# Kernel optimization log

Hardware: AMD Instinct MI355X
Metric: run time of the kernel (lower is better)

## Reference

```python
import jax, jax.numpy as jnp
import numpy as np

B, D, NT, H, K = 4096, 112, 200, 512, 10
HID = 512
IN = 3 * D + NT + 1   # GRU input size = 537
M0 = H + 3 * D + NT   # MLP first-layer input = 1048


def setup_inputs() -> dict:
    key = jax.random.key(0)
    ks = jax.random.split(key, 9)
    def w(k, shape, fan):
        return jax.random.normal(k, shape, jnp.float32) / np.sqrt(fan).astype(np.float32)
    return {
        "z": jax.random.normal(ks[0], (B, D), jnp.float32),
        "c": jax.random.normal(ks[1], (B, D + NT), jnp.float32),
        "b": jax.random.uniform(ks[2], (B, D), jnp.float32),
        "m": jax.random.uniform(ks[3], (B, D), jnp.float32),
        "Wih": w(ks[4], (IN, 3 * H), IN),
        "Whh": w(ks[5], (H, 3 * H), H),
        "bih": jnp.zeros((3 * H,), jnp.float32),
        "bhh": jnp.zeros((3 * H,), jnp.float32),
        "W0": w(ks[6], (M0, HID), M0),
        "b0": jnp.zeros((HID,), jnp.float32),
        "W1": w(ks[7], (HID, HID), HID),
        "b1": jnp.zeros((HID,), jnp.float32),
        "W2": w(ks[8], (HID, 3 * K), HID),
        "b2": jnp.zeros((3 * K,), jnp.float32),
    }


def reference(z, c, b, m, Wih, Whh, bih, bhh, W0, b0, W1, b1, W2, b2):
    """AutoReg.logp: autoregressive GRU + MLP mixture-density head, gaussian base."""
    Bn = z.shape[0]
    const = jnp.concatenate([c, b, m], axis=1)          # [B, 3D+NT] fixed per step
    gi_const = const @ Wih[1:] + bih                    # input-proj of constant part
    w_z = Wih[0]                                        # [3H] weight for scalar z_t
    mlp_const = const @ W0[H:] + b0                     # const part of first MLP layer
    W0h = W0[:H]
    # teacher-forced previous-z sequence: z_0 = -1, then z[:, t-1]
    z_prev = jnp.concatenate([-jnp.ones((Bn, 1), z.dtype), z[:, :-1]], axis=1).T  # [D, B]

    def step(h, zt):  # h: [B,H], zt: [B]
        gi = zt[:, None] * w_z + gi_const               # [B, 3H]
        gh = h @ Whh + bhh
        ir, iz, inn = jnp.split(gi, 3, axis=1)
        hr, hz, hn = jnp.split(gh, 3, axis=1)
        r = jax.nn.sigmoid(ir + hr)
        u = jax.nn.sigmoid(iz + hz)
        n = jnp.tanh(inn + r * hn)
        h2 = (1.0 - u) * n + u * h                      # torch GRU update
        a = jnp.tanh(h2 @ W0h + mlp_const)              # Linear + Tanh on [h||c||b||m]
        a = jnp.tanh(a @ W1 + b1)
        p = a @ W2 + b2                                 # [B, 3K] mixture params
        return h2, p

    h0 = jnp.zeros((Bn, H), z.dtype)
    _, ps = jax.lax.scan(step, h0, z_prev)              # ps: [D, B, 3K]
    params = jnp.transpose(ps, (1, 0, 2))               # [B, D, 3K]

    logits, means, lsig = jnp.split(params, 3, axis=-1)
    sig = jnp.exp(lsig)
    t = z[..., None]
    log_norm = -lsig - 0.5 * np.float32(np.log(2.0 * np.pi))
    log_kern = -0.5 * jnp.square((t - means) / sig)
    ll = jax.nn.logsumexp(log_kern + log_norm + logits, axis=-1) \
         - jax.nn.logsumexp(logits, axis=-1)            # [B, D]

    query = m * (1.0 - b)
    mask = -jnp.sort(-query, axis=1)                    # descending sort values
    return jnp.sum(ll * mask, axis=1)                   # [B]
```

## Files before the change

### kernel.cpp

```cpp
#include <hip/hip_runtime.h>
#include <hip/hip_bf16.h>
#include <float.h>
#include <math.h>

#define BN   4096
#define DD   112
#define HH   512
#define G3   1536
#define CW   536
#define HIDD 512

typedef __attribute__((ext_vector_type(8))) short short8;
typedef __attribute__((ext_vector_type(4))) float float4v;

__device__ __forceinline__ unsigned short f2bf(float x) {
    __hip_bfloat16 h = __float2bfloat16(x);
    return *(unsigned short*)&h;
}

__global__ void build_const(const float* __restrict__ c, const float* __restrict__ b,
                            const float* __restrict__ m, float* __restrict__ out) {
    int idx = blockIdx.x * blockDim.x + threadIdx.x;
    if (idx >= BN * CW) return;
    int row = idx / CW, col = idx - row * CW;
    float v;
    if (col < 312)      v = c[row * 312 + col];
    else if (col < 424) v = b[row * 112 + (col - 312)];
    else                v = m[row * 112 + (col - 424)];
    out[idx] = v;
}

__global__ __launch_bounds__(256) void gemm_bias(const float* __restrict__ A,
        const float* __restrict__ W, const float* __restrict__ bias,
        float* __restrict__ C, int N) {
    __shared__ float As[8][64];
    __shared__ float Ws[8][64];
    const int tid = threadIdx.x;
    const int tx = tid & 15, ty = tid >> 4;
    const int rowBase = blockIdx.x * 64, colBase = blockIdx.y * 64;
    float acc[4][4] = {};
    for (int kb = 0; kb < CW; kb += 8) {
        int l = tid * 2;
        {
            int i = l >> 3, j = l & 7;
            As[j][i] = A[(rowBase + i) * CW + kb + j];
            int i2 = (l + 1) >> 3, j2 = (l + 1) & 7;
            As[j2][i2] = A[(rowBase + i2) * CW + kb + j2];
        }
        {
            int j = l >> 6, n = l & 63;
            Ws[j][n] = W[(kb + j) * N + colBase + n];
            int j2 = (l + 1) >> 6, n2 = (l + 1) & 63;
            Ws[j2][n2] = W[(kb + j2) * N + colBase + n2];
        }
        __syncthreads();
#pragma unroll
        for (int k = 0; k < 8; ++k) {
            float av[4], wv[4];
#pragma unroll
            for (int i = 0; i < 4; ++i) av[i] = As[k][ty * 4 + i];
#pragma unroll
            for (int j = 0; j < 4; ++j) wv[j] = Ws[k][tx * 4 + j];
#pragma unroll
            for (int i = 0; i < 4; ++i)
#pragma unroll
                for (int j = 0; j < 4; ++j) acc[i][j] += av[i] * wv[j];
        }
        __syncthreads();
    }
#pragma unroll
    for (int i = 0; i < 4; ++i) {
        int r = rowBase + ty * 4 + i;
#pragma unroll
        for (int j = 0; j < 4; ++j) {
            int cc = colBase + tx * 4 + j;
            C[r * N + cc] = acc[i][j] + bias[cc];
        }
    }
}

__global__ void sort_mask(const float* __restrict__ b, const float* __restrict__ m,
                          float* __restrict__ maskbuf) {
    __shared__ float s[128];
    const int row = blockIdx.x, t = threadIdx.x;
    float v = -FLT_MAX;
    if (t < DD) v = m[row * DD + t] * (1.0f - b[row * DD + t]);
    s[t] = v;
    __syncthreads();
    for (int k = 2; k <= 128; k <<= 1) {
        for (int j = k >> 1; j > 0; j >>= 1) {
            int ixj = t ^ j;
            if (ixj > t) {
                bool up = ((t & k) == 0);
                float a = s[t], bb = s[ixj];
                if ((a > bb) == up) { s[t] = bb; s[ixj] = a; }
            }
            __syncthreads();
        }
    }
    if (t < DD) maskbuf[row * DD + t] = s[127 - t];
}

__global__ void pack_w(const float* __restrict__ src, unsigned short* __restrict__ dst,
                       int kchunks, int ldn, int ncols) {
    int bid = blockIdx.x;
    int nt = bid / kchunks, kc = bid - nt * kchunks;
    int lane = threadIdx.x;
    int quad = lane >> 4, l16 = lane & 15;
    int n = nt * 16 + l16;
    unsigned short v[8];
#pragma unroll
    for (int j = 0; j < 8; ++j) {
        int k = kc * 32 + quad * 8 + j;
        float f = (n < ncols) ? src[(size_t)k * ldn + n] : 0.0f;
        v[j] = f2bf(f);
    }
    unsigned short* p = dst + ((size_t)bid * 64 + lane) * 8;
#pragma unroll
    for (int j = 0; j < 8; ++j) p[j] = v[j];
}

__global__ __launch_bounds__(1024, 4) void gru_mfma(
    const float* __restrict__ z, const float* __restrict__ Wih,
    const float* __restrict__ bhh, const float* __restrict__ b1,
    const float* __restrict__ b2,
    const float* __restrict__ gi_const, const float* __restrict__ mlp_const,
    const float* __restrict__ maskbuf,
    const unsigned short* __restrict__ WhhP, const unsigned short* __restrict__ W0hP,
    const unsigned short* __restrict__ W1P, const unsigned short* __restrict__ W2P,
    float* __restrict__ out)
{
    __shared__ unsigned short h_bf[16 * 520];
    __shared__ unsigned short a_bf[16 * 520];
    __shared__ float pp[16 * 512];
    __shared__ float zbuf[113 * 16];
    __shared__ float mbuf[16 * 112];

    const int tid = threadIdx.x;
    const int wave = tid >> 6, lane = tid & 63;
    const int quad = lane >> 4, l16 = lane & 15;
    const int pr = tid >> 5, pc = tid & 31;
    const int rowBase = blockIdx.x * 16;

    for (int idx = tid; idx < 16 * 520; idx += 1024) h_bf[idx] = 0;
    for (int idx = tid; idx < 113 * 16; idx += 1024) {
        int tt = idx >> 4, r = idx & 15;
        zbuf[idx] = (tt == 0) ? -1.0f : z[(rowBase + r) * DD + tt - 1];
    }
    for (int idx = tid; idx < 16 * 112; idx += 1024) {
        int r = idx / DD, tt = idx - r * DD;
        mbuf[idx] = maskbuf[(rowBase + r) * DD + tt];
    }

    int hcol[2];
    float wz0[2], wz1[2], wz2[2], bh2r[2], b1c[2];
    float gic0[2][4], gic1[2][4], gic2[2][4], mlc[2][4];
    float h_own[2][4];
#pragma unroll
    for (int i = 0; i < 2; ++i) {
        int tile = wave + 16 * i;
        int hc = tile * 16 + l16;
        hcol[i] = hc;
        wz0[i] = Wih[hc]; wz1[i] = Wih[512 + hc]; wz2[i] = Wih[1024 + hc];
        float bh0 = bhh[hc], bh1 = bhh[512 + hc];
        bh2r[i] = bhh[1024 + hc];
        b1c[i] = b1[hc];
#pragma unroll
        for (int rg = 0; rg < 4; ++rg) {
            int m = quad * 4 + rg;
            const float* g = gi_const + (size_t)(rowBase + m) * G3;
            gic0[i][rg] = g[hc] + bh0;
            gic1[i][rg] = g[512 + hc] + bh1;
            gic2[i][rg] = g[1024 + hc];
            mlc[i][rg] = mlp_const[(size_t)(rowBase + m) * HIDD + hc];
            h_own[i][rg] = 0.0f;
        }
    }
    const float b2v = (pc < 30) ? b2[pc] : 0.0f;
    const int ppbase = (pc >> 4) * 256 + ((pr >> 2) * 16 + (pc & 15)) * 4 + (pr & 3);

    const short8* WhhF = (const short8*)WhhP;
    const short8* W0hF = (const short8*)W0hP;
    const short8* W1F  = (const short8*)W1P;
    const short8* W2F  = (const short8*)W2P;

    float llacc = 0.0f;
    __syncthreads();

    for (int t = 0; t < DD; ++t) {
        float4v accR[2], accU[2], accN[2];
#pragma unroll
        for (int i = 0; i < 2; ++i) {
            accR[i] = (float4v){gic0[i][0], gic0[i][1], gic0[i][2], gic0[i][3]};
            accU[i] = (float4v){gic1[i][0], gic1[i][1], gic1[i][2], gic1[i][3]};
            accN[i] = (float4v){0.f, 0.f, 0.f, 0.f};
        }
#pragma unroll 4
        for (int kc = 0; kc < 16; ++kc) {
            short8 af = *(const short8*)&h_bf[l16 * 520 + kc * 32 + quad * 8];
#pragma unroll
            for (int i = 0; i < 2; ++i) {
                int tile = wave + 16 * i;
                accR[i] = __builtin_amdgcn_mfma_f32_16x16x32_bf16(af, WhhF[(tile * 16 + kc) * 64 + lane], accR[i], 0, 0, 0);
                accU[i] = __builtin_amdgcn_mfma_f32_16x16x32_bf16(af, WhhF[((tile + 32) * 16 + kc) * 64 + lane], accU[i], 0, 0, 0);
                accN[i] = __builtin_amdgcn_mfma_f32_16x16x32_bf16(af, WhhF[((tile + 64) * 16 + kc) * 64 + lane], accN[i], 0, 0, 0);
            }
        }
        __syncthreads();
#pragma unroll
        for (int i = 0; i < 2; ++i) {
#pragma unroll
            for (int rg = 0; rg < 4; ++rg) {
                int m = quad * 4 + rg;
                float zt = zbuf[t * 16 + m];
                float r = 1.0f / (1.0f + __expf(-(accR[i][rg] + zt * wz0[i])));
                float u = 1.0f / (1.0f + __expf(-(accU[i][rg] + zt * wz1[i])));
                float xn = gic2[i][rg] + zt * wz2[i] + r * (accN[i][rg] + bh2r[i]);
                float n = 1.0f - 2.0f / (__expf(2.0f * xn) + 1.0f);
                float h2 = (1.0f - u) * n + u * h_own[i][rg];
                h_own[i][rg] = h2;
                h_bf[m * 520 + hcol[i]] = f2bf(h2);
            }
        }
        __syncthreads();
        float4v acc1[2];
#pragma unroll
        for (int i = 0; i < 2; ++i) acc1[i] = (float4v){mlc[i][0], mlc[i][1], mlc[i][2], mlc[i][3]};
#pragma unroll 4
        for (int kc = 0; kc < 16; ++kc) {
            short8 af = *(const short8*)&h_bf[l16 * 520 + kc * 32 + quad * 8];
#pragma unroll
            for (int i = 0; i < 2; ++i)
                acc1[i] = __builtin_amdgcn_mfma_f32_16x16x32_bf16(af, W0hF[((wave + 16 * i) * 16 + kc) * 64 + lane], acc1[i], 0, 0, 0);
        }
#pragma unroll
        for (int i = 0; i < 2; ++i)
#pragma unroll
            for (int rg = 0; rg < 4; ++rg) {
                int m = quad * 4 + rg;
                float x = acc1[i][rg];
                a_bf[m * 520 + hcol[i]] = f2bf(1.0f - 2.0f / (__expf(2.0f * x) + 1.0f));
            }
        __syncthreads();
        float4v acc2[2];
#pragma unroll
        for (int i = 0; i < 2; ++i) acc2[i] = (float4v){b1c[i], b1c[i], b1c[i], b1c[i]};
#pragma unroll 4
        for (int kc = 0; kc < 16; ++kc) {
            short8 af = *(const short8*)&a_bf[l16 * 520 + kc * 32 + quad * 8];
#pragma unroll
            for (int i = 0; i < 2; ++i)
                acc2[i] = __builtin_amdgcn_mfma_f32_16x16x32_bf16(af, W1F[((wave + 16 * i) * 16 + kc) * 64 + lane], acc2[i], 0, 0, 0);
        }
        __syncthreads();
#pragma unroll
        for (int i = 0; i < 2; ++i)
#pragma unroll
            for (int rg = 0; rg < 4; ++rg) {
                int m = quad * 4 + rg;
                float x = acc2[i][rg];
                a_bf[m * 520 + hcol[i]] = f2bf(1.0f - 2.0f / (__expf(2.0f * x) + 1.0f));
            }
        __syncthreads();
        {
            int kc = wave;
            short8 af = *(const short8*)&a_bf[l16 * 520 + kc * 32 + quad * 8];
            float4v ap0 = (float4v){0.f, 0.f, 0.f, 0.f}, ap1 = (float4v){0.f, 0.f, 0.f, 0.f};
            ap0 = __builtin_amdgcn_mfma_f32_16x16x32_bf16(af, W2F[(0 * 16 + kc) * 64 + lane], ap0, 0, 0, 0);
            ap1 = __builtin_amdgcn_mfma_f32_16x16x32_bf16(af, W2F[(1 * 16 + kc) * 64 + lane], ap1, 0, 0, 0);
#pragma unroll
            for (int rg = 0; rg < 4; ++rg) {
                pp[wave * 512 + 0 * 256 + lane * 4 + rg] = ap0[rg];
                pp[wave * 512 + 1 * 256 + lane * 4 + rg] = ap1[rg];
            }
        }
        __syncthreads();
        if (wave < 8) {
            float pv = b2v;
#pragma unroll
            for (int w = 0; w < 16; ++w) pv += pp[w * 512 + ppbase];
            const int half = lane & 32;
            float meanv = __shfl(pv, half + ((pc + 10) & 31), 64);
            float lsigv = __shfl(pv, half + ((pc + 20) & 31), 64);
            float e1, e2;
            if (pc < 10) {
                float ztar = zbuf[(t + 1) * 16 + pr];
                float invs = __expf(-lsigv);
                float dd = (ztar - meanv) * invs;
                e1 = -0.5f * dd * dd - lsigv - 0.91893853320467274f + pv;
                e2 = pv;
            } else { e1 = -FLT_MAX; e2 = -FLT_MAX; }
            float m1 = e1, m2 = e2;
#pragma unroll
            for (int off = 16; off > 0; off >>= 1) {
                m1 = fmaxf(m1, __shfl_xor(m1, off, 64));
                m2 = fmaxf(m2, __shfl_xor(m2, off, 64));
            }
            float s1 = (pc < 10) ? __expf(e1 - m1) : 0.0f;
            float s2 = (pc < 10) ? __expf(e2 - m2) : 0.0f;
#pragma unroll
            for (int off = 16; off > 0; off >>= 1) {
                s1 += __shfl_xor(s1, off, 64);
                s2 += __shfl_xor(s2, off, 64);
            }
            float ll = (m1 + __logf(s1)) - (m2 + __logf(s2));
            llacc += ll * mbuf[pr * 112 + t];
        }
    }
    if (wave < 8 && pc == 0) out[rowBase + pr] = llacc;
}

extern "C" void kernel_launch(void* const* d_in, const int* in_sizes, int n_in,
                              void* d_out, int out_size, void* d_ws, size_t ws_size,
                              hipStream_t stream) {
    const float* z   = (const float*)d_in[0];
    const float* c   = (const float*)d_in[1];
    const float* b   = (const float*)d_in[2];
    const float* m   = (const float*)d_in[3];
    const float* Wih = (const float*)d_in[4];
    const float* Whh = (const float*)d_in[5];
    const float* bih = (const float*)d_in[6];
    const float* bhh = (const float*)d_in[7];
    const float* W0  = (const float*)d_in[8];
    const float* b0  = (const float*)d_in[9];
    const float* W1  = (const float*)d_in[10];
    const float* b1  = (const float*)d_in[11];
    const float* W2  = (const float*)d_in[12];
    const float* b2  = (const float*)d_in[13];
    float* out = (float*)d_out;

    float* ws        = (float*)d_ws;
    float* constbuf  = ws;
    float* gi_const  = constbuf + (size_t)BN * CW;
    float* mlp_const = gi_const + (size_t)BN * G3;
    float* maskbuf   = mlp_const + (size_t)BN * HIDD;
    unsigned short* WhhP = (unsigned short*)(maskbuf + (size_t)BN * DD);
    unsigned short* W0hP = WhhP + (size_t)96 * 16 * 512;
    unsigned short* W1P  = W0hP + (size_t)32 * 16 * 512;
    unsigned short* W2P  = W1P  + (size_t)32 * 16 * 512;

    build_const<<<(BN * CW + 255) / 256, 256, 0, stream>>>(c, b, m, constbuf);
    dim3 g1(BN / 64, G3 / 64);
    gemm_bias<<<g1, 256, 0, stream>>>(constbuf, Wih + G3, bih, gi_const, G3);
    dim3 g2(BN / 64, HIDD / 64);
    gemm_bias<<<g2, 256, 0, stream>>>(constbuf, W0 + (size_t)HH * HIDD, b0, mlp_const, HIDD);
    sort_mask<<<BN, 128, 0, stream>>>(b, m, maskbuf);

    pack_w<<<96 * 16, 64, 0, stream>>>(Whh, WhhP, 16, G3, G3);
    pack_w<<<32 * 16, 64, 0, stream>>>(W0,  W0hP, 16, HIDD, HIDD);
    pack_w<<<32 * 16, 64, 0, stream>>>(W1,  W1P,  16, HIDD, HIDD);
    pack_w<<<2 * 16, 64, 0, stream>>>(W2,  W2P,  16, 30, 30);

    gru_mfma<<<BN / 16, 1024, 0, stream>>>(z, Wih, bhh, b1, b2, gi_const, mlp_const,
                                           maskbuf, WhhP, W0hP, W1P, W2P, out);
}
```

Measured before the change: 3.149 ms.

## Batch MLP head over two GRU timesteps to reuse weight fragments

The MLP head no longer depends on the recurrence, so the kernel now runs two GRU steps back to back into ping-pong hidden buffers. It then evaluates the MLP layers for both timesteps together, with each loaded W0h/W1 fragment feeding two MFMAs. The W2 projection and the mixture log-likelihood are split across all 16 waves, covering two timesteps, and partial sums are merged at the end. This halves global/L2 weight traffic and the barrier count for the MLP stages. The cost is more registers and LDS, plus an extra barrier per iteration.

```diff
diff --git a/kernel.cpp b/kernel.cpp
--- a/kernel.cpp
+++ b/kernel.cpp
@@ -130,8 +130,9 @@
     const unsigned short* __restrict__ W1P, const unsigned short* __restrict__ W2P,
     float* __restrict__ out)
 {
-    __shared__ unsigned short h_bf[16 * 520];
-    __shared__ unsigned short a_bf[16 * 520];
+    __shared__ unsigned short h_bf0[16 * 520];
+    __shared__ unsigned short h_bf1[16 * 520];
+    __shared__ unsigned short a_bf[32 * 520];
     __shared__ float pp[16 * 512];
     __shared__ float zbuf[113 * 16];
     __shared__ float mbuf[16 * 112];
@@ -142,7 +143,7 @@
     const int pr = tid >> 5, pc = tid & 31;
     const int rowBase = blockIdx.x * 16;
 
-    for (int idx = tid; idx < 16 * 520; idx += 1024) h_bf[idx] = 0;
+    for (int idx = tid; idx < 16 * 520; idx += 1024) h_bf0[idx] = 0;
     for (int idx = tid; idx < 113 * 16; idx += 1024) {
         int tt = idx >> 4, r = idx & 15;
         zbuf[idx] = (tt == 0) ? -1.0f : z[(rowBase + r) * DD + tt - 1];
@@ -177,7 +178,9 @@
         }
     }
     const float b2v = (pc < 30) ? b2[pc] : 0.0f;
-    const int ppbase = (pc >> 4) * 256 + ((pr >> 2) * 16 + (pc & 15)) * 4 + (pr & 3);
+    const int mdn_mt = pr >> 4, mdn_m = pr & 15;
+    const int ppofs = (mdn_mt * 8) * 512 + (pc >> 4) * 256
+                      + ((mdn_m >> 2) * 16 + (pc & 15)) * 4 + (mdn_m & 3);
 
     const short8* WhhF = (const short8*)WhhP;
     const short8* W0hF = (const short8*)W0hP;
@@ -187,87 +190,113 @@
     float llacc = 0.0f;
     __syncthreads();
 
-    for (int t = 0; t < DD; ++t) {
-        float4v accR[2], accU[2], accN[2];
-#pragma unroll
-        for (int i = 0; i < 2; ++i) {
-            accR[i] = (float4v){gic0[i][0], gic0[i][1], gic0[i][2], gic0[i][3]};
-            accU[i] = (float4v){gic1[i][0], gic1[i][1], gic1[i][2], gic1[i][3]};
-            accN[i] = (float4v){0.f, 0.f, 0.f, 0.f};
-        }
+    for (int t = 0; t < DD; t += 2) {
+#pragma unroll
+        for (int step = 0; step < 2; ++step) {
+            const unsigned short* hsrc = step == 0 ? h_bf0 : h_bf1;
+            unsigned short* hdst = step == 0 ? h_bf1 : h_bf0;
+            float4v accR[2], accU[2], accN[2];
+#pragma unroll
+            for (int i = 0; i < 2; ++i) {
+                accR[i] = (float4v){gic0[i][0], gic0[i][1], gic0[i][2], gic0[i][3]};
+                accU[i] = (float4v){gic1[i][0], gic1[i][1], gic1[i][2], gic1[i][3]};
+                accN[i] = (float4v){0.f, 0.f, 0.f, 0.f};
+            }
+#pragma unroll 4
+            for (int kc = 0; kc < 16; ++kc) {
+                short8 af = *(const short8*)&hsrc[l16 * 520 + kc * 32 + quad * 8];
+#pragma unroll
+                for (int i = 0; i < 2; ++i) {
+                    int tile = wave + 16 * i;
+                    accR[i] = __builtin_amdgcn_mfma_f32_16x16x32_bf16(af, WhhF[(tile * 16 + kc) * 64 + lane], accR[i], 0, 0, 0);
+                    accU[i] = __builtin_amdgcn_mfma_f32_16x16x32_bf16(af, WhhF[((tile + 32) * 16 + kc) * 64 + lane], accU[i], 0, 0, 0);
+                    accN[i] = __builtin_amdgcn_mfma_f32_16x16x32_bf16(af, WhhF[((tile + 64) * 16 + kc) * 64 + lane], accN[i], 0, 0, 0);
+                }
+            }
+#pragma unroll
+            for (int i = 0; i < 2; ++i) {
+#pragma unroll
+                for (int rg = 0; rg < 4; ++rg) {
+                    int m = quad * 4 + rg;
+                    float zt = zbuf[(t + step) * 16 + m];
+                    float r = 1.0f / (1.0f + __expf(-(accR[i][rg] + zt * wz0[i])));
+                    float u = 1.0f / (1.0f + __expf(-(accU[i][rg] + zt * wz1[i])));
+                    float xn = gic2[i][rg] + zt * wz2[i] + r * (accN[i][rg] + bh2r[i]);
+                    float n = 1.0f - 2.0f / (__expf(2.0f * xn) + 1.0f);
+                    float h2 = (1.0f - u) * n + u * h_own[i][rg];
+                    h_own[i][rg] = h2;
+                    hdst[m * 520 + hcol[i]] = f2bf(h2);
+                }
+            }
+            __syncthreads();
+        }
+        float4v acc1[2][2];
+#pragma unroll
+        for (int i = 0; i < 2; ++i)
+#pragma unroll
+            for (int mt = 0; mt < 2; ++mt)
+                acc1[i][mt] = (float4v){mlc[i][0], mlc[i][1], mlc[i][2], mlc[i][3]};
 #pragma unroll 4
         for (int kc = 0; kc < 16; ++kc) {
-            short8 af = *(const short8*)&h_bf[l16 * 520 + kc * 32 + quad * 8];
+            short8 af0 = *(const short8*)&h_bf1[l16 * 520 + kc * 32 + quad * 8];
+            short8 af1 = *(const short8*)&h_bf0[l16 * 520 + kc * 32 + quad * 8];
 #pragma unroll
             for (int i = 0; i < 2; ++i) {
-                int tile = wave + 16 * i;
-                accR[i] = __builtin_amdgcn_mfma_f32_16x16x32_bf16(af, WhhF[(tile * 16 + kc) * 64 + lane], accR[i], 0, 0, 0);
-                accU[i] = __builtin_amdgcn_mfma_f32_16x16x32_bf16(af, WhhF[((tile + 32) * 16 + kc) * 64 + lane], accU[i], 0, 0, 0);
-                accN[i] = __builtin_amdgcn_mfma_f32_16x16x32_bf16(af, WhhF[((tile + 64) * 16 + kc) * 64 + lane], accN[i], 0, 0, 0);
-            }
-        }
-        __syncthreads();
-#pragma unroll
-        for (int i = 0; i < 2; ++i) {
-#pragma unroll
-            for (int rg = 0; rg < 4; ++rg) {
-                int m = quad * 4 + rg;
-                float zt = zbuf[t * 16 + m];
-                float r = 1.0f / (1.0f + __expf(-(accR[i][rg] + zt * wz0[i])));
-                float u = 1.0f / (1.0f + __expf(-(accU[i][rg] + zt * wz1[i])));
-                float xn = gic2[i][rg] + zt * wz2[i] + r * (accN[i][rg] + bh2r[i]);
-                float n = 1.0f - 2.0f / (__expf(2.0f * xn) + 1.0f);
-                float h2 = (1.0f - u) * n + u * h_own[i][rg];
-                h_own[i][rg] = h2;
-                h_bf[m * 520 + hcol[i]] = f2bf(h2);
-            }
-        }
-        __syncthreads();
-        float4v acc1[2];
-#pragma unroll
-        for (int i = 0; i < 2; ++i) acc1[i] = (float4v){mlc[i][0], mlc[i][1], mlc[i][2], mlc[i][3]};
+                short8 bf = W0hF[((wave + 16 * i) * 16 + kc) * 64 + lane];
+                acc1[i][0] = __builtin_amdgcn_mfma_f32_16x16x32_bf16(af0, bf, acc1[i][0], 0, 0, 0);
+                acc1[i][1] = __builtin_amdgcn_mfma_f32_16x16x32_bf16(af1, bf, acc1[i][1], 0, 0, 0);
+            }
+        }
+#pragma unroll
+        for (int i = 0; i < 2; ++i)
+#pragma unroll
+            for (int mt = 0; mt < 2; ++mt)
+#pragma unroll
+                for (int rg = 0; rg < 4; ++rg) {
+                    int m = quad * 4 + rg;
+                    float x = acc1[i][mt][rg];
+                    a_bf[(mt * 16 + m) * 520 + hcol[i]] = f2bf(1.0f - 2.0f / (__expf(2.0f * x) + 1.0f));
+                }
+        __syncthreads();
+        float4v acc2[2][2];
+#pragma unroll
+        for (int i = 0; i < 2; ++i)
+#pragma unroll
+            for (int mt = 0; mt < 2; ++mt)
+                acc2[i][mt] = (float4v){b1c[i], b1c[i], b1c[i], b1c[i]};
 #pragma unroll 4
         for (int kc = 0; kc < 16; ++kc) {
-            short8 af = *(const short8*)&h_bf[l16 * 520 + kc * 32 + quad * 8];
-#pragma unroll
-            for (int i = 0; i < 2; ++i)
-                acc1[i] = __builtin_amdgcn_mfma_f32_16x16x32_bf16(af, W0hF[((wave + 16 * i) * 16 + kc) * 64 + lane], acc1[i], 0, 0, 0);
-        }
+            short8 af0 = *(const short8*)&a_bf[l16 * 520 + kc * 32 + quad * 8];
+            short8 af1 = *(const short8*)&a_bf[(16 + l16) * 520 + kc * 32 + quad * 8];
+#pragma unroll
+            for (int i = 0; i < 2; ++i) {
+                short8 bf = W1F[((wave + 16 * i) * 16 + kc) * 64 + lane];
+                acc2[i][0] = __builtin_amdgcn_mfma_f32_16x16x32_bf16(af0, bf, acc2[i][0], 0, 0, 0);
+                acc2[i][1] = __builtin_amdgcn_mfma_f32_16x16x32_bf16(af1, bf, acc2[i][1], 0, 0, 0);
+            }
+        }
+        __syncthreads();
 #pragma unroll
         for (int i = 0; i < 2; ++i)
 #pragma unroll
-            for (int rg = 0; rg < 4; ++rg) {
-                int m = quad * 4 + rg;
-                float x = acc1[i][rg];
-                a_bf[m * 520 + hcol[i]] = f2bf(1.0f - 2.0f / (__expf(2.0f * x) + 1.0f));
-            }
-        __syncthreads();
-        float4v acc2[2];
-#pragma unroll
-        for (int i = 0; i < 2; ++i) acc2[i] = (float4v){b1c[i], b1c[i], b1c[i], b1c[i]};
-#pragma unroll 4
-        for (int kc = 0; kc < 16; ++kc) {
-            short8 af = *(const short8*)&a_bf[l16 * 520 + kc * 32 + quad * 8];
-#pragma unroll
-            for (int i = 0; i < 2; ++i)
-                acc2[i] = __builtin_amdgcn_mfma_f32_16x16x32_bf16(af, W1F[((wave + 16 * i) * 16 + kc) * 64 + lane], acc2[i], 0, 0, 0);
-        }
-        __syncthreads();
-#pragma unroll
-        for (int i = 0; i < 2; ++i)
-#pragma unroll
-            for (int rg = 0; rg < 4; ++rg) {
-                int m = quad * 4 + rg;
-                float x = acc2[i][rg];
-                a_bf[m * 520 + hcol[i]] = f2bf(1.0f - 2.0f / (__expf(2.0f * x) + 1.0f));
-            }
+            for (int mt = 0; mt < 2; ++mt)
+#pragma unroll
+                for (int rg = 0; rg < 4; ++rg) {
+                    int m = quad * 4 + rg;
+                    float x = acc2[i][mt][rg];
+                    a_bf[(mt * 16 + m) * 520 + hcol[i]] = f2bf(1.0f - 2.0f / (__expf(2.0f * x) + 1.0f));
+                }
         __syncthreads();
         {
-            int kc = wave;
-            short8 af = *(const short8*)&a_bf[l16 * 520 + kc * 32 + quad * 8];
+            const int mtw = wave >> 3;
             float4v ap0 = (float4v){0.f, 0.f, 0.f, 0.f}, ap1 = (float4v){0.f, 0.f, 0.f, 0.f};
-            ap0 = __builtin_amdgcn_mfma_f32_16x16x32_bf16(af, W2F[(0 * 16 + kc) * 64 + lane], ap0, 0, 0, 0);
-            ap1 = __builtin_amdgcn_mfma_f32_16x16x32_bf16(af, W2F[(1 * 16 + kc) * 64 + lane], ap1, 0, 0, 0);
+#pragma unroll
+            for (int kk = 0; kk < 2; ++kk) {
+                int kc = (wave & 7) * 2 + kk;
+                short8 af = *(const short8*)&a_bf[(mtw * 16 + l16) * 520 + kc * 32 + quad * 8];
+                ap0 = __builtin_amdgcn_mfma_f32_16x16x32_bf16(af, W2F[(0 * 16 + kc) * 64 + lane], ap0, 0, 0, 0);
+                ap1 = __builtin_amdgcn_mfma_f32_16x16x32_bf16(af, W2F[(1 * 16 + kc) * 64 + lane], ap1, 0, 0, 0);
+            }
 #pragma unroll
             for (int rg = 0; rg < 4; ++rg) {
                 pp[wave * 512 + 0 * 256 + lane * 4 + rg] = ap0[rg];
@@ -275,16 +304,16 @@
             }
         }
         __syncthreads();
-        if (wave < 8) {
+        {
             float pv = b2v;
 #pragma unroll
-            for (int w = 0; w < 16; ++w) pv += pp[w * 512 + ppbase];
+            for (int w = 0; w < 8; ++w) pv += pp[ppofs + w * 512];
             const int half = lane & 32;
             float meanv = __shfl(pv, half + ((pc + 10) & 31), 64);
             float lsigv = __shfl(pv, half + ((pc + 20) & 31), 64);
             float e1, e2;
             if (pc < 10) {
-                float ztar = zbuf[(t + 1) * 16 + pr];
+                float ztar = zbuf[(t + mdn_mt + 1) * 16 + mdn_m];
                 float invs = __expf(-lsigv);
                 float dd = (ztar - meanv) * invs;
                 e1 = -0.5f * dd * dd - lsigv - 0.91893853320467274f + pv;
@@ -304,10 +333,13 @@
                 s2 += __shfl_xor(s2, off, 64);
             }
             float ll = (m1 + __logf(s1)) - (m2 + __logf(s2));
-            llacc += ll * mbuf[pr * 112 + t];
-        }
-    }
-    if (wave < 8 && pc == 0) out[rowBase + pr] = llacc;
+            llacc += ll * mbuf[mdn_m * 112 + t + mdn_mt];
+        }
+        __syncthreads();
+    }
+    if (pc == 0) pp[pr] = llacc;
+    __syncthreads();
+    if (tid < 16) out[rowBase + tid] = pp[tid] + pp[16 + tid];
 }
 
 extern "C" void kernel_launch(void* const* d_in, const int* in_sizes, int n_in,
```

Result: slower. 4.530 ms (+43.9%).

## Split GRU recurrence from MLP head and batch head over time steps

Applied to the files above, without the earlier changes.

Splits the fused per-step kernel into two. A recurrence-only kernel handles 32 rows per block, reuses each Whh fragment across two M-tiles, reads pre-swizzled gate constants (with bhh folded in) and writes bf16 hidden states to a workspace buffer. A separate head kernel then runs the MLP and mixture-density log-likelihood on all timesteps in parallel, accumulating into the output with atomics. This takes the serial MLP work off the recurrence's critical path and raises parallelism, at the cost of about 470MB of extra global traffic for the hidden states, a workspace-size-dependent fallback, and float atomics that make the summation order nondeterministic.

```diff
diff --git a/kernel.cpp b/kernel.cpp
--- a/kernel.cpp
+++ b/kernel.cpp
@@ -79,6 +79,62 @@
     }
 }
 
+__global__ __launch_bounds__(256) void gemm_gicP(const float* __restrict__ A,
+        const float* __restrict__ W, const float* __restrict__ bih,
+        const float* __restrict__ bhh, float* __restrict__ gicP) {
+    const int N = G3;
+    __shared__ float As[8][64];
+    __shared__ float Ws[8][64];
+    const int tid = threadIdx.x;
+    const int tx = tid & 15, ty = tid >> 4;
+    const int rowBase = blockIdx.x * 64, colBase = blockIdx.y * 64;
+    float acc[4][4] = {};
+    for (int kb = 0; kb < CW; kb += 8) {
+        int l = tid * 2;
+        {
+            int i = l >> 3, j = l & 7;
+            As[j][i] = A[(rowBase + i) * CW + kb + j];
+            int i2 = (l + 1) >> 3, j2 = (l + 1) & 7;
+            As[j2][i2] = A[(rowBase + i2) * CW + kb + j2];
+        }
+        {
+            int j = l >> 6, n = l & 63;
+            Ws[j][n] = W[(kb + j) * N + colBase + n];
+            int j2 = (l + 1) >> 6, n2 = (l + 1) & 63;
+            Ws[j2][n2] = W[(kb + j2) * N + colBase + n2];
+        }
+        __syncthreads();
+#pragma unroll
+        for (int k = 0; k < 8; ++k) {
+            float av[4], wv[4];
+#pragma unroll
+            for (int i = 0; i < 4; ++i) av[i] = As[k][ty * 4 + i];
+#pragma unroll
+            for (int j = 0; j < 4; ++j) wv[j] = Ws[k][tx * 4 + j];
+#pragma unroll
+            for (int i = 0; i < 4; ++i)
+#pragma unroll
+                for (int j = 0; j < 4; ++j) acc[i][j] += av[i] * wv[j];
+        }
+        __syncthreads();
+    }
+#pragma unroll
+    for (int i = 0; i < 4; ++i) {
+        int r = rowBase + ty * 4 + i;
+        int ablock = r >> 5, mrem = r & 31, mt = mrem >> 4, mm = mrem & 15;
+        int quad = mm >> 2, rg = mm & 3;
+#pragma unroll
+        for (int j = 0; j < 4; ++j) {
+            int cc = colBase + tx * 4 + j;
+            int g = cc >> 9, nrem = cc & 511, tile = nrem >> 4, l16 = nrem & 15;
+            int wv = tile & 15, ii = tile >> 4;
+            size_t off = ((((size_t)(ablock * 16 + wv) * 2 + ii) * 2 + mt) * 3 + g) * 256
+                         + (quad * 16 + l16) * 4 + rg;
+            gicP[off] = acc[i][j] + bih[cc] + ((g < 2) ? bhh[cc] : 0.0f);
+        }
+    }
+}
+
 __global__ void sort_mask(const float* __restrict__ b, const float* __restrict__ m,
                           float* __restrict__ maskbuf) {
     __shared__ float s[128];
@@ -120,7 +176,270 @@
     for (int j = 0; j < 8; ++j) p[j] = v[j];
 }
 
-__global__ __launch_bounds__(1024, 4) void gru_mfma(
+__global__ __launch_bounds__(1024, 4) void gru_rec(
+    const float* __restrict__ z, const float* __restrict__ Wih,
+    const float* __restrict__ bhh, const float* __restrict__ gicP,
+    const unsigned short* __restrict__ WhhP, unsigned short* __restrict__ h2g)
+{
+    __shared__ unsigned short h_bf[32 * 520];
+    __shared__ float zbuf[113 * 32];
+
+    const int tid = threadIdx.x;
+    const int wave = tid >> 6, lane = tid & 63;
+    const int quad = lane >> 4, l16 = lane & 15;
+    const int rowBase = blockIdx.x * 32;
+
+    for (int idx = tid; idx < 32 * 520; idx += 1024) h_bf[idx] = 0;
+    for (int idx = tid; idx < 113 * 32; idx += 1024) {
+        int tt = idx >> 5, r = idx & 31;
+        zbuf[idx] = (tt == 0) ? -1.0f : z[(size_t)(rowBase + r) * DD + tt - 1];
+    }
+
+    int hcol[2];
+    float wz0[2], wz1[2], wz2[2], bh2r[2];
+#pragma unroll
+    for (int i = 0; i < 2; ++i) {
+        int hc = (wave + 16 * i) * 16 + l16;
+        hcol[i] = hc;
+        wz0[i] = Wih[hc]; wz1[i] = Wih[512 + hc]; wz2[i] = Wih[1024 + hc];
+        bh2r[i] = bhh[1024 + hc];
+    }
+    float h_own[2][2][4];
+#pragma unroll
+    for (int i = 0; i < 2; ++i)
+#pragma unroll
+        for (int mt = 0; mt < 2; ++mt)
+#pragma unroll
+            for (int rg = 0; rg < 4; ++rg) h_own[i][mt][rg] = 0.0f;
+
+    const float* gicW = gicP + (size_t)(blockIdx.x * 16 + wave) * 12 * 256;
+    const short8* WhhF = (const short8*)WhhP;
+    __syncthreads();
+
+    for (int t = 0; t < DD; ++t) {
+        float4v acc[3][2][2];
+#pragma unroll
+        for (int i = 0; i < 2; ++i)
+#pragma unroll
+            for (int mt = 0; mt < 2; ++mt) {
+                acc[0][i][mt] = *(const float4v*)(gicW + ((i * 2 + mt) * 3 + 0) * 256 + lane * 4);
+                acc[1][i][mt] = *(const float4v*)(gicW + ((i * 2 + mt) * 3 + 1) * 256 + lane * 4);
+                acc[2][i][mt] = (float4v){0.f, 0.f, 0.f, 0.f};
+            }
+#pragma unroll 4
+        for (int kc = 0; kc < 16; ++kc) {
+            short8 af[2];
+#pragma unroll
+            for (int mt = 0; mt < 2; ++mt)
+                af[mt] = *(const short8*)&h_bf[(mt * 16 + l16) * 520 + kc * 32 + quad * 8];
+#pragma unroll
+            for (int i = 0; i < 2; ++i) {
+                int tile = wave + 16 * i;
+#pragma unroll
+                for (int g = 0; g < 3; ++g) {
+                    short8 bf = WhhF[((tile + 32 * g) * 16 + kc) * 64 + lane];
+#pragma unroll
+                    for (int mt = 0; mt < 2; ++mt)
+                        acc[g][i][mt] = __builtin_amdgcn_mfma_f32_16x16x32_bf16(af[mt], bf, acc[g][i][mt], 0, 0, 0);
+                }
+            }
+        }
+        __syncthreads();
+#pragma unroll
+        for (int i = 0; i < 2; ++i)
+#pragma unroll
+            for (int mt = 0; mt < 2; ++mt) {
+                float4v gn = *(const float4v*)(gicW + ((i * 2 + mt) * 3 + 2) * 256 + lane * 4);
+#pragma unroll
+                for (int rg = 0; rg < 4; ++rg) {
+                    int m = mt * 16 + quad * 4 + rg;
+                    float zt = zbuf[t * 32 + m];
+                    float r = 1.0f / (1.0f + __expf(-(acc[0][i][mt][rg] + zt * wz0[i])));
+                    float u = 1.0f / (1.0f + __expf(-(acc[1][i][mt][rg] + zt * wz1[i])));
+                    float xn = gn[rg] + zt * wz2[i] + r * (acc[2][i][mt][rg] + bh2r[i]);
+                    float n = 1.0f - 2.0f / (__expf(2.0f * xn) + 1.0f);
+                    float h2 = (1.0f - u) * n + u * h_own[i][mt][rg];
+                    h_own[i][mt][rg] = h2;
+                    h_bf[m * 520 + hcol[i]] = f2bf(h2);
+                }
+            }
+        __syncthreads();
+        {
+            int flat = tid * 16;
+            int r = flat >> 9, col = flat & 511;
+            const uint4* src = (const uint4*)&h_bf[r * 520 + col];
+            uint4 v0 = src[0], v1 = src[1];
+            uint4* dst = (uint4*)&h2g[((size_t)(rowBase + r) * DD + t) * 512 + col];
+            dst[0] = v0; dst[1] = v1;
+        }
+    }
+}
+
+__global__ __launch_bounds__(1024, 4) void head_mdn(
+    const float* __restrict__ z, const float* __restrict__ b1,
+    const float* __restrict__ b2, const float* __restrict__ mlp_const,
+    const float* __restrict__ maskbuf, const unsigned short* __restrict__ h2g,
+    const unsigned short* __restrict__ W0hP, const unsigned short* __restrict__ W1P,
+    const unsigned short* __restrict__ W2P, float* __restrict__ out)
+{
+    __shared__ unsigned short h_bf[32 * 520];
+    __shared__ unsigned short a_bf[32 * 520];
+    __shared__ float pp[16 * 512];
+
+    const int tid = threadIdx.x;
+    const int wave = tid >> 6, lane = tid & 63;
+    const int quad = lane >> 4, l16 = lane & 15;
+    const int pr = tid >> 5, pc = tid & 31;
+    const int bi = blockIdx.x / 7, ti = blockIdx.x - bi * 7;
+    const int b0 = bi * 2, t0 = ti * 16;
+
+    {
+        int flat = tid * 16;
+        int r = flat >> 9, col = flat & 511;
+        int bb = b0 + (r >> 4), tt = t0 + (r & 15);
+        const uint4* src = (const uint4*)&h2g[((size_t)bb * DD + tt) * 512 + col];
+        uint4 v0 = src[0], v1 = src[1];
+        uint4* dst = (uint4*)&h_bf[r * 520 + col];
+        dst[0] = v0; dst[1] = v1;
+    }
+    int hcol[2];
+    float b1c[2], mlc[2][2];
+#pragma unroll
+    for (int i = 0; i < 2; ++i) {
+        int hc = (wave + 16 * i) * 16 + l16;
+        hcol[i] = hc;
+        b1c[i] = b1[hc];
+#pragma unroll
+        for (int mt = 0; mt < 2; ++mt) mlc[i][mt] = mlp_const[(size_t)(b0 + mt) * HIDD + hc];
+    }
+    const float b2v = (pc < 30) ? b2[pc] : 0.0f;
+    const int mdn_mt = pr >> 4, mdn_m = pr & 15;
+    const int ppofs = (mdn_mt * 8) * 512 + (pc >> 4) * 256
+                      + ((mdn_m >> 2) * 16 + (pc & 15)) * 4 + (mdn_m & 3);
+
+    const short8* W0hF = (const short8*)W0hP;
+    const short8* W1F  = (const short8*)W1P;
+    const short8* W2F  = (const short8*)W2P;
+    __syncthreads();
+
+    float4v acc1[2][2];
+#pragma unroll
+    for (int i = 0; i < 2; ++i)
+#pragma unroll
+        for (int mt = 0; mt < 2; ++mt)
+            acc1[i][mt] = (float4v){mlc[i][mt], mlc[i][mt], mlc[i][mt], mlc[i][mt]};
+#pragma unroll 4
+    for (int kc = 0; kc < 16; ++kc) {
+        short8 af0 = *(const short8*)&h_bf[l16 * 520 + kc * 32 + quad * 8];
+        short8 af1 = *(const short8*)&h_bf[(16 + l16) * 520 + kc * 32 + quad * 8];
+#pragma unroll
+        for (int i = 0; i < 2; ++i) {
+            short8 bf = W0hF[((wave + 16 * i) * 16 + kc) * 64 + lane];
+            acc1[i][0] = __builtin_amdgcn_mfma_f32_16x16x32_bf16(af0, bf, acc1[i][0], 0, 0, 0);
+            acc1[i][1] = __builtin_amdgcn_mfma_f32_16x16x32_bf16(af1, bf, acc1[i][1], 0, 0, 0);
+        }
+    }
+#pragma unroll
+    for (int i = 0; i < 2; ++i)
+#pragma unroll
+        for (int mt = 0; mt < 2; ++mt)
+#pragma unroll
+            for (int rg = 0; rg < 4; ++rg) {
+                int m = mt * 16 + quad * 4 + rg;
+                float x = acc1[i][mt][rg];
+                a_bf[m * 520 + hcol[i]] = f2bf(1.0f - 2.0f / (__expf(2.0f * x) + 1.0f));
+            }
+    __syncthreads();
+    float4v acc2[2][2];
+#pragma unroll
+    for (int i = 0; i < 2; ++i)
+#pragma unroll
+        for (int mt = 0; mt < 2; ++mt)
+            acc2[i][mt] = (float4v){b1c[i], b1c[i], b1c[i], b1c[i]};
+#pragma unroll 4
+    for (int kc = 0; kc < 16; ++kc) {
+        short8 af0 = *(const short8*)&a_bf[l16 * 520 + kc * 32 + quad * 8];
+        short8 af1 = *(const short8*)&a_bf[(16 + l16) * 520 + kc * 32 + quad * 8];
+#pragma unroll
+        for (int i = 0; i < 2; ++i) {
+            short8 bf = W1F[((wave + 16 * i) * 16 + kc) * 64 + lane];
+            acc2[i][0] = __builtin_amdgcn_mfma_f32_16x16x32_bf16(af0, bf, acc2[i][0], 0, 0, 0);
+            acc2[i][1] = __builtin_amdgcn_mfma_f32_16x16x32_bf16(af1, bf, acc2[i][1], 0, 0, 0);
+        }
+    }
+    __syncthreads();
+#pragma unroll
+    for (int i = 0; i < 2; ++i)
+#pragma unroll
+        for (int mt = 0; mt < 2; ++mt)
+#pragma unroll
+            for (int rg = 0; rg < 4; ++rg) {
+                int m = mt * 16 + quad * 4 + rg;
+                float x = acc2[i][mt][rg];
+                a_bf[m * 520 + hcol[i]] = f2bf(1.0f - 2.0f / (__expf(2.0f * x) + 1.0f));
+            }
+    __syncthreads();
+    {
+        const int mtw = wave >> 3;
+        float4v ap0 = (float4v){0.f, 0.f, 0.f, 0.f}, ap1 = (float4v){0.f, 0.f, 0.f, 0.f};
+#pragma unroll
+        for (int kk = 0; kk < 2; ++kk) {
+            int kc = (wave & 7) * 2 + kk;
+            short8 af = *(const short8*)&a_bf[(mtw * 16 + l16) * 520 + kc * 32 + quad * 8];
+            ap0 = __builtin_amdgcn_mfma_f32_16x16x32_bf16(af, W2F[(0 * 16 + kc) * 64 + lane], ap0, 0, 0, 0);
+            ap1 = __builtin_amdgcn_mfma_f32_16x16x32_bf16(af, W2F[(1 * 16 + kc) * 64 + lane], ap1, 0, 0, 0);
+        }
+#pragma unroll
+        for (int rg = 0; rg < 4; ++rg) {
+            pp[wave * 512 + 0 * 256 + lane * 4 + rg] = ap0[rg];
+            pp[wave * 512 + 1 * 256 + lane * 4 + rg] = ap1[rg];
+        }
+    }
+    __syncthreads();
+    float llm;
+    {
+        float pv = b2v;
+#pragma unroll
+        for (int w = 0; w < 8; ++w) pv += pp[ppofs + w * 512];
+        const int half = lane & 32;
+        float meanv = __shfl(pv, half + ((pc + 10) & 31), 64);
+        float lsigv = __shfl(pv, half + ((pc + 20) & 31), 64);
+        float e1, e2;
+        if (pc < 10) {
+            float ztar = z[(size_t)(b0 + mdn_mt) * DD + t0 + mdn_m];
+            float invs = __expf(-lsigv);
+            float dd = (ztar - meanv) * invs;
+            e1 = -0.5f * dd * dd - lsigv - 0.91893853320467274f + pv;
+            e2 = pv;
+        } else { e1 = -FLT_MAX; e2 = -FLT_MAX; }
+        float m1 = e1, m2 = e2;
+#pragma unroll
+        for (int off = 16; off > 0; off >>= 1) {
+            m1 = fmaxf(m1, __shfl_xor(m1, off, 64));
+            m2 = fmaxf(m2, __shfl_xor(m2, off, 64));
+        }
+        float s1 = (pc < 10) ? __expf(e1 - m1) : 0.0f;
+        float s2 = (pc < 10) ? __expf(e2 - m2) : 0.0f;
+#pragma unroll
+        for (int off = 16; off > 0; off >>= 1) {
+            s1 += __shfl_xor(s1, off, 64);
+            s2 += __shfl_xor(s2, off, 64);
+        }
+        float ll = (m1 + __logf(s1)) - (m2 + __logf(s2));
+        llm = ll * maskbuf[(size_t)(b0 + mdn_mt) * DD + t0 + mdn_m];
+    }
+    __syncthreads();
+    if (pc == 0) pp[pr] = llm;
+    __syncthreads();
+    if (tid < 2) {
+        float s = 0.0f;
+#pragma unroll
+        for (int j = 0; j < 16; ++j) s += pp[tid * 16 + j];
+        atomicAdd(&out[b0 + tid], s);
+    }
+}
+
+__global__ __launch_bounds__(1024, 4) void gru_mfma_r5(
     const float* __restrict__ z, const float* __restrict__ Wih,
     const float* __restrict__ bhh, const float* __restrict__ b1,
     const float* __restrict__ b2,
@@ -151,7 +470,6 @@
         int r = idx / DD, tt = idx - r * DD;
         mbuf[idx] = maskbuf[(rowBase + r) * DD + tt];
     }
-
     int hcol[2];
     float wz0[2], wz1[2], wz2[2], bh2r[2], b1c[2];
     float gic0[2][4], gic1[2][4], gic2[2][4], mlc[2][4];
@@ -178,15 +496,12 @@
     }
     const float b2v = (pc < 30) ? b2[pc] : 0.0f;
     const int ppbase = (pc >> 4) * 256 + ((pr >> 2) * 16 + (pc & 15)) * 4 + (pr & 3);
-
     const short8* WhhF = (const short8*)WhhP;
     const short8* W0hF = (const short8*)W0hP;
     const short8* W1F  = (const short8*)W1P;
     const short8* W2F  = (const short8*)W2P;
-
     float llacc = 0.0f;
     __syncthreads();
-
     for (int t = 0; t < DD; ++t) {
         float4v accR[2], accU[2], accN[2];
 #pragma unroll
@@ -331,26 +646,39 @@
 
     float* ws        = (float*)d_ws;
     float* constbuf  = ws;
-    float* gi_const  = constbuf + (size_t)BN * CW;
-    float* mlp_const = gi_const + (size_t)BN * G3;
+    float* gi_region = constbuf + (size_t)BN * CW;
+    float* mlp_const = gi_region + (size_t)BN * G3;
     float* maskbuf   = mlp_const + (size_t)BN * HIDD;
     unsigned short* WhhP = (unsigned short*)(maskbuf + (size_t)BN * DD);
     unsigned short* W0hP = WhhP + (size_t)96 * 16 * 512;
     unsigned short* W1P  = W0hP + (size_t)32 * 16 * 512;
     unsigned short* W2P  = W1P  + (size_t)32 * 16 * 512;
+    unsigned short* h2g  = W2P + (size_t)2 * 16 * 512;
+
+    const size_t need = (size_t)(constbuf ? 0 : 0)
+        + ((size_t)BN * (CW + G3 + HIDD + DD)) * 4
+        + ((size_t)(96 + 32 + 32 + 2) * 16 * 512) * 2
+        + (size_t)BN * DD * 512 * 2;
 
     build_const<<<(BN * CW + 255) / 256, 256, 0, stream>>>(c, b, m, constbuf);
-    dim3 g1(BN / 64, G3 / 64);
-    gemm_bias<<<g1, 256, 0, stream>>>(constbuf, Wih + G3, bih, gi_const, G3);
     dim3 g2(BN / 64, HIDD / 64);
     gemm_bias<<<g2, 256, 0, stream>>>(constbuf, W0 + (size_t)HH * HIDD, b0, mlp_const, HIDD);
     sort_mask<<<BN, 128, 0, stream>>>(b, m, maskbuf);
-
     pack_w<<<96 * 16, 64, 0, stream>>>(Whh, WhhP, 16, G3, G3);
     pack_w<<<32 * 16, 64, 0, stream>>>(W0,  W0hP, 16, HIDD, HIDD);
     pack_w<<<32 * 16, 64, 0, stream>>>(W1,  W1P,  16, HIDD, HIDD);
     pack_w<<<2 * 16, 64, 0, stream>>>(W2,  W2P,  16, 30, 30);
 
-    gru_mfma<<<BN / 16, 1024, 0, stream>>>(z, Wih, bhh, b1, b2, gi_const, mlp_const,
-                                           maskbuf, WhhP, W0hP, W1P, W2P, out);
-}
+    dim3 g1(BN / 64, G3 / 64);
+    if (ws_size >= need) {
+        gemm_gicP<<<g1, 256, 0, stream>>>(constbuf, Wih + G3, bih, bhh, gi_region);
+        hipMemsetAsync(d_out, 0, (size_t)out_size * sizeof(float), stream);
+        gru_rec<<<BN / 32, 1024, 0, stream>>>(z, Wih, bhh, gi_region, WhhP, h2g);
+        head_mdn<<<(BN / 2) * (DD / 16), 1024, 0, stream>>>(z, b1, b2, mlp_const,
+                                                            maskbuf, h2g, W0hP, W1P, W2P, out);
+    } else {
+        gemm_bias<<<g1, 256, 0, stream>>>(constbuf, Wih + G3, bih, gi_region, G3);
+        gru_mfma_r5<<<BN / 16, 1024, 0, stream>>>(z, Wih, bhh, b1, b2, gi_region,
+                                                  mlp_const, maskbuf, WhhP, W0hP, W1P, W2P, out);
+    }
+}
```

New measurement: 3.152 ms. Within noise of the previous version (+0.1%).
